# Optimization experiments

Measured on AMD Instinct MI355X. Metric: run time of the kernel, lower is better.

## Reference

```python
import jax, jax.numpy as jnp
import numpy as np

N = 50000        # nodes
E = 1_600_000    # edges (avg degree 32)
G = 512          # graphs
F_IN = 9         # node features
H = 64           # hidden dim
ED = 1           # edge feature dim


def _lin(k, fo, fi):
    w = jax.random.normal(k, (fo, fi), jnp.float32) * (1.0 / np.sqrt(fi))
    b = jnp.zeros((fo,), jnp.float32)
    return w, b


def setup_inputs() -> dict:
    key = jax.random.key(0)
    ks = jax.random.split(key, 16)
    x = jax.random.normal(ks[0], (N, F_IN), jnp.float32)
    edge_index = jax.random.randint(ks[1], (2, E), 0, N, dtype=jnp.int64)
    edge_attr = jax.random.normal(ks[2], (E, ED), jnp.float32)
    batch = jnp.sort(jax.random.randint(ks[3], (N,), 0, G, dtype=jnp.int64))
    B_total = jax.random.uniform(ks[4], (G,), jnp.float32) * 100.0
    terminal_mask = jax.random.randint(ks[5], (N,), 0, 2, dtype=jnp.int32)
    c_cost = jax.random.uniform(ks[6], (N,), jnp.float32)
    # conv1: edge lin (ED->F_IN), nn = Linear(F_IN,H), Linear(H,H)
    e1_w, e1_b = _lin(ks[7], F_IN, ED)
    w1a, b1a = _lin(ks[8], H, F_IN)
    w1b, b1b = _lin(ks[9], H, H)
    # conv2: edge lin (ED->H), nn = Linear(H,H), Linear(H,H)
    e2_w, e2_b = _lin(ks[10], H, ED)
    w2a, b2a = _lin(ks[11], H, H)
    w2b, b2b = _lin(ks[12], H, H)
    # readout: Linear(H,H//2), Linear(H//2,1)
    wr1, br1 = _lin(ks[13], H // 2, H)
    wr2, br2 = _lin(ks[14], 1, H // 2)
    return dict(x=x, edge_index=edge_index, edge_attr=edge_attr, batch=batch,
                B_total=B_total, terminal_mask=terminal_mask, c_cost=c_cost,
                e1_w=e1_w, e1_b=e1_b, w1a=w1a, b1a=b1a, w1b=w1b, b1b=b1b,
                e2_w=e2_w, e2_b=e2_b, w2a=w2a, b2a=b2a, w2b=w2b, b2b=b2b,
                wr1=wr1, br1=br1, wr2=wr2, br2=br2)


def _gine(x, src, dst, edge_attr, ew, eb, wa, ba, wb, bb):
    # GINEConv (eps=0): nn(x + sum_j relu(x_j + W_e e_ji))
    e = edge_attr @ ew.T + eb                    # [E, F]
    m = jax.nn.relu(x[src] + e)                  # [E, F] gather + edge fuse
    aggr = jax.ops.segment_sum(m, dst, num_segments=N)  # scatter-add -> [N, F]
    h = x + aggr
    h = jax.nn.relu(h @ wa.T + ba)
    h = jax.nn.relu(h @ wb.T + bb)
    return h


def reference(x, edge_index, edge_attr, batch, B_total, terminal_mask, c_cost,
              e1_w, e1_b, w1a, b1a, w1b, b1b,
              e2_w, e2_b, w2a, b2a, w2b, b2b,
              wr1, br1, wr2, br2):
    src, dst = edge_index[0], edge_index[1]
    h = _gine(x, src, dst, edge_attr, e1_w, e1_b, w1a, b1a, w1b, b1b)
    h = _gine(h, src, dst, edge_attr, e2_w, e2_b, w2a, b2a, w2b, b2b)
    pi_raw = jax.nn.sigmoid((jax.nn.relu(h @ wr1.T + br1) @ wr2.T + br2))[:, 0]
    pi_raw = pi_raw * (1.0 - terminal_mask.astype(jnp.float32))
    node_expenses = pi_raw * c_cost
    total_expenses = jax.ops.segment_sum(node_expenses, batch, num_segments=G)
    ratio = jnp.minimum(B_total[batch] / (total_expenses[batch] + 1e-12), 1.0)
    return pi_raw * ratio
```

## Files before the change

### kernel.cpp

```cpp
#include <hip/hip_runtime.h>
#include <hip/hip_fp16.h>
#include <math.h>

#define N_NODES 50000
#define N_EDGES 1600000
#define N_GRAPHS 512
#define F_IN 9
#define H 64
#define EPB 4096
#define N_SBLK ((N_EDGES + EPB - 1) / EPB)
#define BUCKET_NODES 64
#define N_FBUK ((N_NODES + BUCKET_NODES - 1) / BUCKET_NODES)
#define FCAP 2816

typedef _Float16 f16x8 __attribute__((ext_vector_type(8)));
typedef float f32x4 __attribute__((ext_vector_type(4)));
typedef float f32x2 __attribute__((ext_vector_type(2)));

__device__ __forceinline__ void pack_weights_body(
        const float* __restrict__ w1a, const float* __restrict__ w1b,
        const float* __restrict__ w2a, const float* __restrict__ w2b,
        const float* __restrict__ wr1,
        __half* __restrict__ pk1Ah, __half* __restrict__ pk1Al,
        __half* __restrict__ pk1Bh, __half* __restrict__ pk1Bl,
        __half* __restrict__ pkAh, __half* __restrict__ pkAl,
        __half* __restrict__ pkBh, __half* __restrict__ pkBl,
        __half* __restrict__ pkRh, __half* __restrict__ pkRl) {
    int t = threadIdx.x;
    for (int i = t; i < 2048; i += 512) {
        int j = i & 7, l = (i >> 3) & 63, tt = i >> 9;
        int q = l >> 4, n = l & 15;
        int k = q * 8 + j;
        float v = (k < F_IN) ? w1a[(tt * 16 + n) * F_IN + k] : 0.f;
        __half h = __float2half(v);
        pk1Ah[i] = h; pk1Al[i] = __float2half(v - __half2float(h));
    }
    for (int i = t; i < 4096; i += 512) {
        int j = i & 7, l = (i >> 3) & 63, c = (i >> 9) & 1, tt = i >> 10;
        int q = l >> 4, n = l & 15;
        int src = (tt * 16 + n) * H + c * 32 + q * 8 + j;
        float v1 = w1b[src], wa = w2a[src], wb = w2b[src];
        __half h1 = __float2half(v1), ah = __float2half(wa), bh = __float2half(wb);
        pk1Bh[i] = h1; pk1Bl[i] = __float2half(v1 - __half2float(h1));
        pkAh[i] = ah; pkAl[i] = __float2half(wa - __half2float(ah));
        pkBh[i] = bh; pkBl[i] = __float2half(wb - __half2float(bh));
    }
    for (int i = t; i < 2048; i += 512) {
        int j = i & 7, l = (i >> 3) & 63, c = (i >> 9) & 1, tt = i >> 10;
        int q = l >> 4, n = l & 15;
        float wr = wr1[(tt * 16 + n) * H + c * 32 + q * 8 + j];
        __half rh = __float2half(wr);
        pkRh[i] = rh; pkRl[i] = __float2half(wr - __half2float(rh));
    }
}

__global__ void __launch_bounds__(512)
bucket_scatter(const int* __restrict__ ei,
               const float* __restrict__ ea,
               int* __restrict__ bnext,
               uint2* __restrict__ ebuk,
               const float* __restrict__ w1a,
               const float* __restrict__ w1b,
               const float* __restrict__ w2a,
               const float* __restrict__ w2b,
               const float* __restrict__ wr1,
               __half* pk1Ah, __half* pk1Al,
               __half* pk1Bh, __half* pk1Bl,
               __half* pkAh, __half* pkAl,
               __half* pkBh, __half* pkBl,
               __half* pkRh, __half* pkRl) {
    if (blockIdx.x == 0) {
        pack_weights_body(w1a, w1b, w2a, w2b, wr1, pk1Ah, pk1Al, pk1Bh, pk1Bl,
                          pkAh, pkAl, pkBh, pkBl, pkRh, pkRl);
        return;
    }
    __shared__ int cnt[N_FBUK];
    __shared__ int gbase[N_FBUK];
    for (int i = threadIdx.x; i < N_FBUK; i += 512) cnt[i] = 0;
    __syncthreads();
    int base = (blockIdx.x - 1) * EPB;
    int rk[8];
    unsigned pay[8];
#pragma unroll
    for (int j = 0; j < 8; ++j) {
        int e = base + j * 512 + threadIdx.x;
        rk[j] = -1;
        if (e < N_EDGES) {
            int d = ei[N_EDGES + e];
            int s = ei[e];
            float a = ea[e];
            pay[j] = ((unsigned)s << 16) |
                     (unsigned)__half_as_ushort(__float2half(a));
            int b = d >> 6;
            int r = atomicAdd(&cnt[b], 1);
            rk[j] = (b << 19) | ((d & 63) << 13) | r;
        }
    }
    __syncthreads();
    for (int i = threadIdx.x; i < N_FBUK; i += 512)
        gbase[i] = cnt[i] ? atomicAdd(&bnext[i], cnt[i]) : 0;
    __syncthreads();
#pragma unroll
    for (int j = 0; j < 8; ++j) {
        if (rk[j] < 0) continue;
        int b = rk[j] >> 19, dl = (rk[j] >> 13) & 63, r = rk[j] & 8191;
        int slot = gbase[b] + r;
        if (slot >= FCAP) continue;
        ebuk[(size_t)b * FCAP + slot] = make_uint2(pay[j], (unsigned)dl);
    }
}

#define UNPACK_ATTR(P) __half2float(__ushort_as_half((unsigned short)((P) & 0xffffu)))

__device__ __forceinline__ void split8(const float* __restrict__ v,
                                       f16x8& hi, f16x8& lo) {
#pragma unroll
    for (int j = 0; j < 8; ++j) {
        _Float16 h = (_Float16)v[j];
        hi[j] = h;
        lo[j] = (_Float16)(v[j] - (float)h);
    }
}

#define TILE3(C, A0H, A0L, A1H, A1L, PH, PL, T) do {                          \
        f16x8 b0h = *(const f16x8*)((PH) + (((T) * 2 + 0) * 64 + lane) * 8);  \
        f16x8 b0l = *(const f16x8*)((PL) + (((T) * 2 + 0) * 64 + lane) * 8);  \
        f16x8 b1h = *(const f16x8*)((PH) + (((T) * 2 + 1) * 64 + lane) * 8);  \
        f16x8 b1l = *(const f16x8*)((PL) + (((T) * 2 + 1) * 64 + lane) * 8);  \
        C = __builtin_amdgcn_mfma_f32_16x16x32_f16(A0H, b0h, C, 0, 0, 0);     \
        C = __builtin_amdgcn_mfma_f32_16x16x32_f16(A0L, b0h, C, 0, 0, 0);     \
        C = __builtin_amdgcn_mfma_f32_16x16x32_f16(A0H, b0l, C, 0, 0, 0);     \
        C = __builtin_amdgcn_mfma_f32_16x16x32_f16(A1H, b1h, C, 0, 0, 0);     \
        C = __builtin_amdgcn_mfma_f32_16x16x32_f16(A1L, b1h, C, 0, 0, 0);     \
        C = __builtin_amdgcn_mfma_f32_16x16x32_f16(A1H, b1l, C, 0, 0, 0);     \
    } while (0)

__global__ void __launch_bounds__(512)
bucket_fine(const uint2* __restrict__ ebuk,
            const int* __restrict__ bnext,
            unsigned* __restrict__ ep4,
            int* __restrict__ starts, int* __restrict__ deg,
            const float* __restrict__ x,
            const float* __restrict__ e1w,
            const float* __restrict__ e1b,
            const __half* __restrict__ pk1Ah, const __half* __restrict__ pk1Al,
            const float* __restrict__ b1a,
            const __half* __restrict__ pk1Bh, const __half* __restrict__ pk1Bl,
            const float* __restrict__ b1b,
            __half* __restrict__ h1) {
    __shared__ unsigned sorted[FCAP];
    __shared__ int cntN[BUCKET_NODES], offN[BUCKET_NODES], nxtN[BUCKET_NODES];
    __shared__ float xs_lds[BUCKET_NODES][32];
    __shared__ float hbuf[4][16][68];
    int b = blockIdx.x;
    int base = b * FCAP;
    int count = bnext[b];
    if (count > FCAP) count = FCAP;
    int tid = threadIdx.x;
    if (tid < BUCKET_NODES) cntN[tid] = 0;
    __syncthreads();
    uint2 ev[6];
#pragma unroll
    for (int k = 0; k < 6; ++k) {
        int i = tid + k * 512;
        ev[k] = (i < count) ? ebuk[base + i] : make_uint2(0u, 0xFFFFFFFFu);
    }
#pragma unroll
    for (int k = 0; k < 6; ++k)
        if (ev[k].y < (unsigned)BUCKET_NODES) atomicAdd(&cntN[ev[k].y], 1);
    __syncthreads();
    if (tid < 64) {
        int v = cntN[tid];
        int incl = v;
#pragma unroll
        for (int off = 1; off < 64; off <<= 1) {
            int t = __shfl_up(incl, off, 64);
            if (tid >= off) incl += t;
        }
        int excl = incl - v;
        offN[tid] = excl;
        nxtN[tid] = 0;
        int n = (b << 6) + tid;
        if (n < N_NODES) { starts[n] = base + excl; deg[n] = v; }
    }
    __syncthreads();
#pragma unroll
    for (int k = 0; k < 6; ++k) {
        if (ev[k].y < (unsigned)BUCKET_NODES) {
            int r = atomicAdd(&nxtN[ev[k].y], 1);
            sorted[offN[ev[k].y] + r] = ev[k].x;
        }
    }
    __syncthreads();
    for (int i = tid; i < count; i += 512)
        ep4[base + i] = sorted[i];

    int lane = tid & 63, wid = tid >> 6;
    int slot = lane >> 4;
    int f = lane & 15;
    bool act = f < F_IN;
    float wf = act ? e1w[f] : 0.f;
    float bf = act ? e1b[f] : 0.f;
#pragma unroll
    for (int i = 0; i < 8; ++i) {
        int nloc = wid * 8 + i;
        int n = (b << 6) + nloc;
        bool valid = (n < N_NODES);
        int off = offN[nloc];
        int dgN = valid ? cntN[nloc] : 0;
        float acc = 0.f;
        int j = slot;
        for (; j + 12 < dgN; j += 16) {
            unsigned pa = sorted[off + j];
            unsigned pb = sorted[off + j + 4];
            unsigned pc = sorted[off + j + 8];
            unsigned pd = sorted[off + j + 12];
            float xa_ = act ? x[(pa >> 16) * F_IN + f] : 0.f;
            float xb_ = act ? x[(pb >> 16) * F_IN + f] : 0.f;
            float xc_ = act ? x[(pc >> 16) * F_IN + f] : 0.f;
            float xd_ = act ? x[(pd >> 16) * F_IN + f] : 0.f;
            if (act) {
                acc += fmaxf(xa_ + UNPACK_ATTR(pa) * wf + bf, 0.f)
                     + fmaxf(xb_ + UNPACK_ATTR(pb) * wf + bf, 0.f)
                     + fmaxf(xc_ + UNPACK_ATTR(pc) * wf + bf, 0.f)
                     + fmaxf(xd_ + UNPACK_ATTR(pd) * wf + bf, 0.f);
            }
        }
        for (; j < dgN; j += 4) {
            unsigned p = sorted[off + j];
            float xv = act ? x[(p >> 16) * F_IN + f] : 0.f;
            float m = xv + UNPACK_ATTR(p) * wf + bf;
            acc += act ? fmaxf(m, 0.f) : 0.f;
        }
        acc += __shfl_xor(acc, 16, 64);
        acc += __shfl_xor(acc, 32, 64);
        if (lane < 32) {
            float o = 0.f;
            if (valid && lane < F_IN) o = x[n * F_IN + lane] + acc;
            xs_lds[nloc][lane] = o;
        }
    }
    __syncthreads();

    bool mlpw = (wid < 4);
    int m = lane & 15, q = lane >> 4;
    const _Float16* pAh = (const _Float16*)pk1Ah;
    const _Float16* pAl = (const _Float16*)pk1Al;
    const _Float16* pBh = (const _Float16*)pk1Bh;
    const _Float16* pBl = (const _Float16*)pk1Bl;
    if (mlpw) {
        f16x8 ah, al;
        split8(&xs_lds[wid * 16 + m][q * 8], ah, al);
#pragma unroll
        for (int t = 0; t < 4; ++t) {
            f32x4 c = {0.f, 0.f, 0.f, 0.f};
            f16x8 bh = *(const f16x8*)(pAh + (t * 64 + lane) * 8);
            f16x8 bl = *(const f16x8*)(pAl + (t * 64 + lane) * 8);
            c = __builtin_amdgcn_mfma_f32_16x16x32_f16(ah, bh, c, 0, 0, 0);
            c = __builtin_amdgcn_mfma_f32_16x16x32_f16(al, bh, c, 0, 0, 0);
            c = __builtin_amdgcn_mfma_f32_16x16x32_f16(ah, bl, c, 0, 0, 0);
            float bias = b1a[t * 16 + m];
#pragma unroll
            for (int r = 0; r < 4; ++r)
                hbuf[wid][q * 4 + r][t * 16 + m] = fmaxf(c[r] + bias, 0.f);
        }
    }
    __syncthreads();
    if (mlpw) {
        f16x8 a0h, a0l, a1h, a1l;
        split8(&hbuf[wid][m][q * 8], a0h, a0l);
        split8(&hbuf[wid][m][32 + q * 8], a1h, a1l);
        float tmp[4][4];
#pragma unroll
        for (int t = 0; t < 4; ++t) {
            f32x4 c = {0.f, 0.f, 0.f, 0.f};
            TILE3(c, a0h, a0l, a1h, a1l, pBh, pBl, t);
            float bias = b1b[t * 16 + m];
#pragma unroll
            for (int r = 0; r < 4; ++r)
                tmp[t][r] = fmaxf(c[r] + bias, 0.f);
        }
        __builtin_amdgcn_s_barrier();
#pragma unroll
        for (int t = 0; t < 4; ++t)
#pragma unroll
            for (int r = 0; r < 4; ++r)
                hbuf[wid][q * 4 + r][t * 16 + m] = tmp[t][r];
        int nn = lane >> 2, part = lane & 3;
        int n = (b << 6) + wid * 16 + nn;
        if (n < N_NODES) {
            f16x8 vlo, vhi;
            const float* rlo = &hbuf[wid][nn][part * 8];
            const float* rhi = &hbuf[wid][nn][32 + part * 8];
#pragma unroll
            for (int j = 0; j < 8; ++j) {
                vlo[j] = (_Float16)rlo[j];
                vhi[j] = (_Float16)rhi[j];
            }
            *(f16x8*)(h1 + (size_t)n * 64 + part * 8) = vlo;
            *(f16x8*)(h1 + (size_t)n * 64 + 32 + part * 8) = vhi;
        }
    }
}

__global__ void aggphase2_kernel(const __half* __restrict__ h1,
                                 const int* __restrict__ starts,
                                 const int* __restrict__ deg,
                                 const unsigned* __restrict__ ep4,
                                 const float* __restrict__ ew,
                                 const float* __restrict__ eb,
                                 float* __restrict__ htot) {
    int n = blockIdx.x * (blockDim.x >> 6) + (threadIdx.x >> 6);
    int lane = threadIdx.x & 63;
    if (n >= N_NODES) return;
    int q = lane >> 4;
    int l = lane & 15;
    int s0 = starts[n], dg = deg[n];
    const unsigned* ep = ep4 + s0;
    const uint2* h1v = (const uint2*)h1;
    float4 w4 = *(const float4*)(ew + 4 * l);
    float4 b4 = *(const float4*)(eb + 4 * l);
    float a0 = 0.f, a1 = 0.f, a2 = 0.f, a3 = 0.f;
#define EDGE4(P, V) do {                                                   \
        float at = UNPACK_ATTR(P);                                         \
        float2 lo = __half22float2(*(const __half2*)&(V).x);               \
        float2 hi = __half22float2(*(const __half2*)&(V).y);               \
        a0 += fmaxf(lo.x + at * w4.x + b4.x, 0.f);                         \
        a1 += fmaxf(lo.y + at * w4.y + b4.y, 0.f);                         \
        a2 += fmaxf(hi.x + at * w4.z + b4.z, 0.f);                         \
        a3 += fmaxf(hi.y + at * w4.w + b4.w, 0.f);                         \
    } while (0)
    int j = 0;
    for (; j + 16 <= dg; j += 16) {
        unsigned p0 = ep[j + q], p1 = ep[j + 4 + q];
        unsigned p2 = ep[j + 8 + q], p3 = ep[j + 12 + q];
        uint2 v0 = h1v[(size_t)(p0 >> 16) * 16 + l];
        uint2 v1 = h1v[(size_t)(p1 >> 16) * 16 + l];
        uint2 v2 = h1v[(size_t)(p2 >> 16) * 16 + l];
        uint2 v3 = h1v[(size_t)(p3 >> 16) * 16 + l];
        EDGE4(p0, v0); EDGE4(p1, v1); EDGE4(p2, v2); EDGE4(p3, v3);
    }
    for (; j + 4 <= dg; j += 4) {
        unsigned p = ep[j + q];
        uint2 v = h1v[(size_t)(p >> 16) * 16 + l];
        EDGE4(p, v);
    }
    int rem = dg - j;
    if (q < rem) {
        unsigned p = ep[j + q];
        uint2 v = h1v[(size_t)(p >> 16) * 16 + l];
        EDGE4(p, v);
    }
#undef EDGE4
    a0 += __shfl_xor(a0, 16, 64); a0 += __shfl_xor(a0, 32, 64);
    a1 += __shfl_xor(a1, 16, 64); a1 += __shfl_xor(a1, 32, 64);
    a2 += __shfl_xor(a2, 16, 64); a2 += __shfl_xor(a2, 32, 64);
    a3 += __shfl_xor(a3, 16, 64); a3 += __shfl_xor(a3, 32, 64);
    if (q == 0) {
        uint2 sv = h1v[(size_t)n * 16 + l];
        float2 lo = __half22float2(*(const __half2*)&sv.x);
        float2 hi = __half22float2(*(const __half2*)&sv.y);
        f32x4 o;
        o[0] = lo.x + a0; o[1] = lo.y + a1; o[2] = hi.x + a2; o[3] = hi.y + a3;
        __builtin_nontemporal_store(o, (f32x4*)(htot + (size_t)n * 64 + 4 * l));
    }
}

__global__ void node2_kernel(const float* __restrict__ htot,
                             const __half* __restrict__ pkAh, const __half* __restrict__ pkAl,
                             const float* __restrict__ b2a,
                             const __half* __restrict__ pkBh, const __half* __restrict__ pkBl,
                             const float* __restrict__ b2b,
                             const __half* __restrict__ pkRh, const __half* __restrict__ pkRl,
                             const float* __restrict__ br1,
                             const float* __restrict__ wr2,
                             const float* __restrict__ br2,
                             const int* __restrict__ term,
                             const int* __restrict__ batch,
                             const float* __restrict__ ccost,
                             float* __restrict__ pi,
                             float* __restrict__ te) {
    __shared__ float hbuf[4][16][68];
    int wv = threadIdx.x >> 6;
    int lane = threadIdx.x & 63;
    int gwave = blockIdx.x * 4 + wv;
    bool active = gwave < (N_NODES / 16);
    int base = active ? gwave * 16 : 0;
    int m = lane & 15, q = lane >> 4;
    const _Float16* pAh = (const _Float16*)pkAh;
    const _Float16* pAl = (const _Float16*)pkAl;
    const _Float16* pBh = (const _Float16*)pkBh;
    const _Float16* pBl = (const _Float16*)pkBl;
    const _Float16* pRh = (const _Float16*)pkRh;
    const _Float16* pRl = (const _Float16*)pkRl;

    f16x8 a0h, a0l, a1h, a1l;
    {
        const float* hrow = htot + (size_t)(base + m) * 64;
        split8(hrow + q * 8, a0h, a0l);
        split8(hrow + 32 + q * 8, a1h, a1l);
    }
#pragma unroll
    for (int t = 0; t < 4; ++t) {
        f32x4 c = {0.f, 0.f, 0.f, 0.f};
        TILE3(c, a0h, a0l, a1h, a1l, pAh, pAl, t);
        float bias = b2a[t * 16 + m];
#pragma unroll
        for (int r = 0; r < 4; ++r)
            hbuf[wv][q * 4 + r][t * 16 + m] = fmaxf(c[r] + bias, 0.f);
    }
    __syncthreads();
    split8(&hbuf[wv][m][q * 8], a0h, a0l);
    split8(&hbuf[wv][m][32 + q * 8], a1h, a1l);
    float tmp[4][4];
#pragma unroll
    for (int t = 0; t < 4; ++t) {
        f32x4 c = {0.f, 0.f, 0.f, 0.f};
        TILE3(c, a0h, a0l, a1h, a1l, pBh, pBl, t);
        float bias = b2b[t * 16 + m];
#pragma unroll
        for (int r = 0; r < 4; ++r)
            tmp[t][r] = fmaxf(c[r] + bias, 0.f);
    }
    __syncthreads();
#pragma unroll
    for (int t = 0; t < 4; ++t)
#pragma unroll
        for (int r = 0; r < 4; ++r)
            hbuf[wv][q * 4 + r][t * 16 + m] = tmp[t][r];
    __syncthreads();
    split8(&hbuf[wv][m][q * 8], a0h, a0l);
    split8(&hbuf[wv][m][32 + q * 8], a1h, a1l);
    float partial[4] = {0.f, 0.f, 0.f, 0.f};
#pragma unroll
    for (int t = 0; t < 2; ++t) {
        f32x4 c = {0.f, 0.f, 0.f, 0.f};
        TILE3(c, a0h, a0l, a1h, a1l, pRh, pRl, t);
        float bias = br1[t * 16 + m];
        float wv2 = wr2[t * 16 + m];
#pragma unroll
        for (int r = 0; r < 4; ++r)
            partial[r] += fmaxf(c[r] + bias, 0.f) * wv2;
    }
#pragma unroll
    for (int off = 1; off < 16; off <<= 1) {
        partial[0] += __shfl_xor(partial[0], off, 64);
        partial[1] += __shfl_xor(partial[1], off, 64);
        partial[2] += __shfl_xor(partial[2], off, 64);
        partial[3] += __shfl_xor(partial[3], off, 64);
    }
    if (active && m == 0) {
#pragma unroll
        for (int r = 0; r < 4; ++r) {
            int n = base + q * 4 + r;
            float z = partial[r] + br2[0];
            float sig = 1.f / (1.f + expf(-z));
            float pv = sig * (1.f - (float)term[n]);
            pi[n] = pv;
            float contrib = pv * ccost[n];
            if (contrib != 0.f) atomicAdd(&te[batch[n]], contrib);
        }
    }
}

__global__ void final_kernel(const float* __restrict__ pi,
                             const int* __restrict__ batch,
                             const float* __restrict__ Btot,
                             const float* __restrict__ te,
                             float* __restrict__ out) {
    int n = blockIdx.x * blockDim.x + threadIdx.x;
    if (n >= N_NODES) return;
    int b = batch[n];
    float ratio = fminf(Btot[b] / (te[b] + 1e-12f), 1.f);
    out[n] = pi[n] * ratio;
}

extern "C" void kernel_launch(void* const* d_in, const int* in_sizes, int n_in,
                              void* d_out, int out_size, void* d_ws, size_t ws_size,
                              hipStream_t stream) {
    const float* x     = (const float*)d_in[0];
    const int*   ei    = (const int*)d_in[1];
    const float* ea    = (const float*)d_in[2];
    const int*   batch = (const int*)d_in[3];
    const float* Btot  = (const float*)d_in[4];
    const int*   term  = (const int*)d_in[5];
    const float* ccost = (const float*)d_in[6];
    const float* e1w   = (const float*)d_in[7];
    const float* e1b   = (const float*)d_in[8];
    const float* w1a   = (const float*)d_in[9];
    const float* b1a   = (const float*)d_in[10];
    const float* w1b   = (const float*)d_in[11];
    const float* b1b   = (const float*)d_in[12];
    const float* e2w   = (const float*)d_in[13];
    const float* e2b   = (const float*)d_in[14];
    const float* w2a   = (const float*)d_in[15];
    const float* b2a   = (const float*)d_in[16];
    const float* w2b   = (const float*)d_in[17];
    const float* b2b   = (const float*)d_in[18];
    const float* wr1   = (const float*)d_in[19];
    const float* br1   = (const float*)d_in[20];
    const float* wr2   = (const float*)d_in[21];
    const float* br2   = (const float*)d_in[22];

    char* p = (char*)d_ws;
    int*      bnext  = (int*)p;      p += sizeof(int)      * 1024;
    float*    te     = (float*)p;    p += sizeof(float)    * N_GRAPHS;
    int*      starts = (int*)p;      p += sizeof(int)      * N_NODES;
    int*      deg    = (int*)p;      p += sizeof(int)      * N_NODES;
    p = (char*)(((size_t)p + 15) & ~(size_t)15);
    uint2*    ebuk   = (uint2*)p;    p += sizeof(uint2)    * (size_t)N_FBUK * FCAP;
    unsigned* ep4    = (unsigned*)p; p += sizeof(unsigned) * (size_t)N_FBUK * FCAP;
    __half*   h1     = (__half*)p;   p += sizeof(__half)   * (size_t)N_NODES * 64;
    float*    htot   = (float*)p;    p += sizeof(float)    * (size_t)N_NODES * 64;
    float*    pi     = (float*)p;    p += sizeof(float)    * N_NODES;
    __half*   pk1Ah  = (__half*)p;   p += sizeof(__half)   * 2048;
    __half*   pk1Al  = (__half*)p;   p += sizeof(__half)   * 2048;
    __half*   pk1Bh  = (__half*)p;   p += sizeof(__half)   * 4096;
    __half*   pk1Bl  = (__half*)p;   p += sizeof(__half)   * 4096;
    __half*   pkAh   = (__half*)p;   p += sizeof(__half)   * 4096;
    __half*   pkAl   = (__half*)p;   p += sizeof(__half)   * 4096;
    __half*   pkBh   = (__half*)p;   p += sizeof(__half)   * 4096;
    __half*   pkBl   = (__half*)p;   p += sizeof(__half)   * 4096;
    __half*   pkRh   = (__half*)p;   p += sizeof(__half)   * 2048;
    __half*   pkRl   = (__half*)p;   p += sizeof(__half)   * 2048;
    float*    out    = (float*)d_out;

    hipMemsetAsync(d_ws, 0, sizeof(int) * 1024 + sizeof(float) * N_GRAPHS, stream);

    bucket_scatter<<<1 + N_SBLK, 512, 0, stream>>>(ei, ea, bnext, ebuk,
                                                   w1a, w1b, w2a, w2b, wr1,
                                                   pk1Ah, pk1Al, pk1Bh, pk1Bl,
                                                   pkAh, pkAl, pkBh, pkBl, pkRh, pkRl);
    bucket_fine<<<N_FBUK, 512, 0, stream>>>(ebuk, bnext, ep4, starts, deg,
                                            x, e1w, e1b,
                                            pk1Ah, pk1Al, b1a, pk1Bh, pk1Bl, b1b, h1);
    aggphase2_kernel<<<(N_NODES + 3) / 4, 256, 0, stream>>>(h1, starts, deg, ep4,
                                                            e2w, e2b, htot);
    node2_kernel<<<(N_NODES / 16 + 3) / 4, 256, 0, stream>>>(htot,
                                                             pkAh, pkAl, b2a,
                                                             pkBh, pkBl, b2b,
                                                             pkRh, pkRl, br1,
                                                             wr2, br2, term,
                                                             batch, ccost, pi, te);
    final_kernel<<<(N_NODES + 255) / 256, 256, 0, stream>>>(pi, batch, Btot, te, out);
}
```

Before: 217.3 us.

## Fuse layer-2 aggregation with node MLP and readout via LDS staging

```diff
diff --git a/kernel.cpp b/kernel.cpp
--- a/kernel.cpp
+++ b/kernel.cpp
@@ -264,9 +264,6 @@
             for (int r = 0; r < 4; ++r)
                 hbuf[wid][q * 4 + r][t * 16 + m] = fmaxf(c[r] + bias, 0.f);
         }
-    }
-    __syncthreads();
-    if (mlpw) {
         f16x8 a0h, a0l, a1h, a1l;
         split8(&hbuf[wid][m][q * 8], a0h, a0l);
         split8(&hbuf[wid][m][32 + q * 8], a1h, a1l);
@@ -280,7 +277,6 @@
             for (int r = 0; r < 4; ++r)
                 tmp[t][r] = fmaxf(c[r] + bias, 0.f);
         }
-        __builtin_amdgcn_s_barrier();
 #pragma unroll
         for (int t = 0; t < 4; ++t)
 #pragma unroll
@@ -303,24 +299,35 @@
     }
 }
 
-__global__ void aggphase2_kernel(const __half* __restrict__ h1,
-                                 const int* __restrict__ starts,
-                                 const int* __restrict__ deg,
-                                 const unsigned* __restrict__ ep4,
-                                 const float* __restrict__ ew,
-                                 const float* __restrict__ eb,
-                                 float* __restrict__ htot) {
-    int n = blockIdx.x * (blockDim.x >> 6) + (threadIdx.x >> 6);
-    int lane = threadIdx.x & 63;
-    if (n >= N_NODES) return;
+__global__ void __launch_bounds__(256)
+aggnode2_kernel(const __half* __restrict__ h1,
+                const int* __restrict__ starts,
+                const int* __restrict__ deg,
+                const unsigned* __restrict__ ep4,
+                const float* __restrict__ ew,
+                const float* __restrict__ eb,
+                const __half* __restrict__ pkAh, const __half* __restrict__ pkAl,
+                const float* __restrict__ b2a,
+                const __half* __restrict__ pkBh, const __half* __restrict__ pkBl,
+                const float* __restrict__ b2b,
+                const __half* __restrict__ pkRh, const __half* __restrict__ pkRl,
+                const float* __restrict__ br1,
+                const float* __restrict__ wr2,
+                const float* __restrict__ br2,
+                const int* __restrict__ term,
+                const int* __restrict__ batch,
+                const float* __restrict__ ccost,
+                float* __restrict__ pi,
+                float* __restrict__ te) {
+    __shared__ float htot_lds[16][68];
+    __shared__ float hbuf[16][68];
+    int lane = threadIdx.x & 63, wid = threadIdx.x >> 6;
+    int gbase = blockIdx.x * 16;
     int q = lane >> 4;
     int l = lane & 15;
-    int s0 = starts[n], dg = deg[n];
-    const unsigned* ep = ep4 + s0;
     const uint2* h1v = (const uint2*)h1;
     float4 w4 = *(const float4*)(ew + 4 * l);
     float4 b4 = *(const float4*)(eb + 4 * l);
-    float a0 = 0.f, a1 = 0.f, a2 = 0.f, a3 = 0.f;
 #define EDGE4(P, V) do {                                                   \
         float at = UNPACK_ATTR(P);                                         \
         float2 lo = __half22float2(*(const __half2*)&(V).x);               \
@@ -330,135 +337,118 @@
         a2 += fmaxf(hi.x + at * w4.z + b4.z, 0.f);                         \
         a3 += fmaxf(hi.y + at * w4.w + b4.w, 0.f);                         \
     } while (0)
-    int j = 0;
-    for (; j + 16 <= dg; j += 16) {
-        unsigned p0 = ep[j + q], p1 = ep[j + 4 + q];
-        unsigned p2 = ep[j + 8 + q], p3 = ep[j + 12 + q];
-        uint2 v0 = h1v[(size_t)(p0 >> 16) * 16 + l];
-        uint2 v1 = h1v[(size_t)(p1 >> 16) * 16 + l];
-        uint2 v2 = h1v[(size_t)(p2 >> 16) * 16 + l];
-        uint2 v3 = h1v[(size_t)(p3 >> 16) * 16 + l];
-        EDGE4(p0, v0); EDGE4(p1, v1); EDGE4(p2, v2); EDGE4(p3, v3);
-    }
-    for (; j + 4 <= dg; j += 4) {
-        unsigned p = ep[j + q];
-        uint2 v = h1v[(size_t)(p >> 16) * 16 + l];
-        EDGE4(p, v);
-    }
-    int rem = dg - j;
-    if (q < rem) {
-        unsigned p = ep[j + q];
-        uint2 v = h1v[(size_t)(p >> 16) * 16 + l];
-        EDGE4(p, v);
+#pragma unroll
+    for (int k = 0; k < 4; ++k) {
+        int nloc = wid * 4 + k;
+        int n = gbase + nloc;
+        int s0 = starts[n], dg = deg[n];
+        const unsigned* ep = ep4 + s0;
+        float a0 = 0.f, a1 = 0.f, a2 = 0.f, a3 = 0.f;
+        int j = 0;
+        for (; j + 16 <= dg; j += 16) {
+            unsigned p0 = ep[j + q], p1 = ep[j + 4 + q];
+            unsigned p2 = ep[j + 8 + q], p3 = ep[j + 12 + q];
+            uint2 v0 = h1v[(size_t)(p0 >> 16) * 16 + l];
+            uint2 v1 = h1v[(size_t)(p1 >> 16) * 16 + l];
+            uint2 v2 = h1v[(size_t)(p2 >> 16) * 16 + l];
+            uint2 v3 = h1v[(size_t)(p3 >> 16) * 16 + l];
+            EDGE4(p0, v0); EDGE4(p1, v1); EDGE4(p2, v2); EDGE4(p3, v3);
+        }
+        for (; j + 4 <= dg; j += 4) {
+            unsigned p = ep[j + q];
+            uint2 v = h1v[(size_t)(p >> 16) * 16 + l];
+            EDGE4(p, v);
+        }
+        int rem = dg - j;
+        if (q < rem) {
+            unsigned p = ep[j + q];
+            uint2 v = h1v[(size_t)(p >> 16) * 16 + l];
+            EDGE4(p, v);
+        }
+        a0 += __shfl_xor(a0, 16, 64); a0 += __shfl_xor(a0, 32, 64);
+        a1 += __shfl_xor(a1, 16, 64); a1 += __shfl_xor(a1, 32, 64);
+        a2 += __shfl_xor(a2, 16, 64); a2 += __shfl_xor(a2, 32, 64);
+        a3 += __shfl_xor(a3, 16, 64); a3 += __shfl_xor(a3, 32, 64);
+        if (q == 0) {
+            uint2 sv = h1v[(size_t)n * 16 + l];
+            float2 lo = __half22float2(*(const __half2*)&sv.x);
+            float2 hi = __half22float2(*(const __half2*)&sv.y);
+            f32x4 o;
+            o[0] = lo.x + a0; o[1] = lo.y + a1; o[2] = hi.x + a2; o[3] = hi.y + a3;
+            *(f32x4*)&htot_lds[nloc][4 * l] = o;
+        }
     }
 #undef EDGE4
-    a0 += __shfl_xor(a0, 16, 64); a0 += __shfl_xor(a0, 32, 64);
-    a1 += __shfl_xor(a1, 16, 64); a1 += __shfl_xor(a1, 32, 64);
-    a2 += __shfl_xor(a2, 16, 64); a2 += __shfl_xor(a2, 32, 64);
-    a3 += __shfl_xor(a3, 16, 64); a3 += __shfl_xor(a3, 32, 64);
-    if (q == 0) {
-        uint2 sv = h1v[(size_t)n * 16 + l];
-        float2 lo = __half22float2(*(const __half2*)&sv.x);
-        float2 hi = __half22float2(*(const __half2*)&sv.y);
-        f32x4 o;
-        o[0] = lo.x + a0; o[1] = lo.y + a1; o[2] = hi.x + a2; o[3] = hi.y + a3;
-        __builtin_nontemporal_store(o, (f32x4*)(htot + (size_t)n * 64 + 4 * l));
-    }
-}
-
-__global__ void node2_kernel(const float* __restrict__ htot,
-                             const __half* __restrict__ pkAh, const __half* __restrict__ pkAl,
-                             const float* __restrict__ b2a,
-                             const __half* __restrict__ pkBh, const __half* __restrict__ pkBl,
-                             const float* __restrict__ b2b,
-                             const __half* __restrict__ pkRh, const __half* __restrict__ pkRl,
-                             const float* __restrict__ br1,
-                             const float* __restrict__ wr2,
-                             const float* __restrict__ br2,
-                             const int* __restrict__ term,
-                             const int* __restrict__ batch,
-                             const float* __restrict__ ccost,
-                             float* __restrict__ pi,
-                             float* __restrict__ te) {
-    __shared__ float hbuf[4][16][68];
-    int wv = threadIdx.x >> 6;
-    int lane = threadIdx.x & 63;
-    int gwave = blockIdx.x * 4 + wv;
-    bool active = gwave < (N_NODES / 16);
-    int base = active ? gwave * 16 : 0;
-    int m = lane & 15, q = lane >> 4;
-    const _Float16* pAh = (const _Float16*)pkAh;
-    const _Float16* pAl = (const _Float16*)pkAl;
-    const _Float16* pBh = (const _Float16*)pkBh;
-    const _Float16* pBl = (const _Float16*)pkBl;
-    const _Float16* pRh = (const _Float16*)pkRh;
-    const _Float16* pRl = (const _Float16*)pkRl;
-
-    f16x8 a0h, a0l, a1h, a1l;
-    {
-        const float* hrow = htot + (size_t)(base + m) * 64;
-        split8(hrow + q * 8, a0h, a0l);
-        split8(hrow + 32 + q * 8, a1h, a1l);
-    }
-#pragma unroll
-    for (int t = 0; t < 4; ++t) {
-        f32x4 c = {0.f, 0.f, 0.f, 0.f};
-        TILE3(c, a0h, a0l, a1h, a1l, pAh, pAl, t);
-        float bias = b2a[t * 16 + m];
-#pragma unroll
-        for (int r = 0; r < 4; ++r)
-            hbuf[wv][q * 4 + r][t * 16 + m] = fmaxf(c[r] + bias, 0.f);
-    }
-    __syncthreads();
-    split8(&hbuf[wv][m][q * 8], a0h, a0l);
-    split8(&hbuf[wv][m][32 + q * 8], a1h, a1l);
-    float tmp[4][4];
-#pragma unroll
-    for (int t = 0; t < 4; ++t) {
-        f32x4 c = {0.f, 0.f, 0.f, 0.f};
-        TILE3(c, a0h, a0l, a1h, a1l, pBh, pBl, t);
-        float bias = b2b[t * 16 + m];
-#pragma unroll
-        for (int r = 0; r < 4; ++r)
-            tmp[t][r] = fmaxf(c[r] + bias, 0.f);
-    }
-    __syncthreads();
-#pragma unroll
-    for (int t = 0; t < 4; ++t)
-#pragma unroll
-        for (int r = 0; r < 4; ++r)
-            hbuf[wv][q * 4 + r][t * 16 + m] = tmp[t][r];
-    __syncthreads();
-    split8(&hbuf[wv][m][q * 8], a0h, a0l);
-    split8(&hbuf[wv][m][32 + q * 8], a1h, a1l);
-    float partial[4] = {0.f, 0.f, 0.f, 0.f};
-#pragma unroll
-    for (int t = 0; t < 2; ++t) {
-        f32x4 c = {0.f, 0.f, 0.f, 0.f};
-        TILE3(c, a0h, a0l, a1h, a1l, pRh, pRl, t);
-        float bias = br1[t * 16 + m];
-        float wv2 = wr2[t * 16 + m];
-#pragma unroll
-        for (int r = 0; r < 4; ++r)
-            partial[r] += fmaxf(c[r] + bias, 0.f) * wv2;
-    }
-#pragma unroll
-    for (int off = 1; off < 16; off <<= 1) {
-        partial[0] += __shfl_xor(partial[0], off, 64);
-        partial[1] += __shfl_xor(partial[1], off, 64);
-        partial[2] += __shfl_xor(partial[2], off, 64);
-        partial[3] += __shfl_xor(partial[3], off, 64);
-    }
-    if (active && m == 0) {
-#pragma unroll
-        for (int r = 0; r < 4; ++r) {
-            int n = base + q * 4 + r;
-            float z = partial[r] + br2[0];
-            float sig = 1.f / (1.f + expf(-z));
-            float pv = sig * (1.f - (float)term[n]);
-            pi[n] = pv;
-            float contrib = pv * ccost[n];
-            if (contrib != 0.f) atomicAdd(&te[batch[n]], contrib);
+    __syncthreads();
+
+    if (wid == 0) {
+        int m = lane & 15;
+        const _Float16* pAh = (const _Float16*)pkAh;
+        const _Float16* pAl = (const _Float16*)pkAl;
+        const _Float16* pBh = (const _Float16*)pkBh;
+        const _Float16* pBl = (const _Float16*)pkBl;
+        const _Float16* pRh = (const _Float16*)pkRh;
+        const _Float16* pRl = (const _Float16*)pkRl;
+        f16x8 a0h, a0l, a1h, a1l;
+        split8(&htot_lds[m][q * 8], a0h, a0l);
+        split8(&htot_lds[m][32 + q * 8], a1h, a1l);
+#pragma unroll
+        for (int t = 0; t < 4; ++t) {
+            f32x4 c = {0.f, 0.f, 0.f, 0.f};
+            TILE3(c, a0h, a0l, a1h, a1l, pAh, pAl, t);
+            float bias = b2a[t * 16 + m];
+#pragma unroll
+            for (int r = 0; r < 4; ++r)
+                hbuf[q * 4 + r][t * 16 + m] = fmaxf(c[r] + bias, 0.f);
+        }
+        split8(&hbuf[m][q * 8], a0h, a0l);
+        split8(&hbuf[m][32 + q * 8], a1h, a1l);
+        float tmp[4][4];
+#pragma unroll
+        for (int t = 0; t < 4; ++t) {
+            f32x4 c = {0.f, 0.f, 0.f, 0.f};
+            TILE3(c, a0h, a0l, a1h, a1l, pBh, pBl, t);
+            float bias = b2b[t * 16 + m];
+#pragma unroll
+            for (int r = 0; r < 4; ++r)
+                tmp[t][r] = fmaxf(c[r] + bias, 0.f);
+        }
+#pragma unroll
+        for (int t = 0; t < 4; ++t)
+#pragma unroll
+            for (int r = 0; r < 4; ++r)
+                hbuf[q * 4 + r][t * 16 + m] = tmp[t][r];
+        split8(&hbuf[m][q * 8], a0h, a0l);
+        split8(&hbuf[m][32 + q * 8], a1h, a1l);
+        float partial[4] = {0.f, 0.f, 0.f, 0.f};
+#pragma unroll
+        for (int t = 0; t < 2; ++t) {
+            f32x4 c = {0.f, 0.f, 0.f, 0.f};
+            TILE3(c, a0h, a0l, a1h, a1l, pRh, pRl, t);
+            float bias = br1[t * 16 + m];
+            float wv2 = wr2[t * 16 + m];
+#pragma unroll
+            for (int r = 0; r < 4; ++r)
+                partial[r] += fmaxf(c[r] + bias, 0.f) * wv2;
+        }
+#pragma unroll
+        for (int off = 1; off < 16; off <<= 1) {
+            partial[0] += __shfl_xor(partial[0], off, 64);
+            partial[1] += __shfl_xor(partial[1], off, 64);
+            partial[2] += __shfl_xor(partial[2], off, 64);
+            partial[3] += __shfl_xor(partial[3], off, 64);
+        }
+        if (m == 0) {
+#pragma unroll
+            for (int r = 0; r < 4; ++r) {
+                int n = gbase + q * 4 + r;
+                float z = partial[r] + br2[0];
+                float sig = 1.f / (1.f + expf(-z));
+                float pv = sig * (1.f - (float)term[n]);
+                pi[n] = pv;
+                float contrib = pv * ccost[n];
+                if (contrib != 0.f) atomicAdd(&te[batch[n]], contrib);
+            }
         }
     }
 }
@@ -511,7 +501,6 @@
     uint2*    ebuk   = (uint2*)p;    p += sizeof(uint2)    * (size_t)N_FBUK * FCAP;
     unsigned* ep4    = (unsigned*)p; p += sizeof(unsigned) * (size_t)N_FBUK * FCAP;
     __half*   h1     = (__half*)p;   p += sizeof(__half)   * (size_t)N_NODES * 64;
-    float*    htot   = (float*)p;    p += sizeof(float)    * (size_t)N_NODES * 64;
     float*    pi     = (float*)p;    p += sizeof(float)    * N_NODES;
     __half*   pk1Ah  = (__half*)p;   p += sizeof(__half)   * 2048;
     __half*   pk1Al  = (__half*)p;   p += sizeof(__half)   * 2048;
@@ -534,13 +523,12 @@
     bucket_fine<<<N_FBUK, 512, 0, stream>>>(ebuk, bnext, ep4, starts, deg,
                                             x, e1w, e1b,
                                             pk1Ah, pk1Al, b1a, pk1Bh, pk1Bl, b1b, h1);
-    aggphase2_kernel<<<(N_NODES + 3) / 4, 256, 0, stream>>>(h1, starts, deg, ep4,
-                                                            e2w, e2b, htot);
-    node2_kernel<<<(N_NODES / 16 + 3) / 4, 256, 0, stream>>>(htot,
-                                                             pkAh, pkAl, b2a,
-                                                             pkBh, pkBl, b2b,
-                                                             pkRh, pkRl, br1,
-                                                             wr2, br2, term,
-                                                             batch, ccost, pi, te);
+    aggnode2_kernel<<<N_NODES / 16, 256, 0, stream>>>(h1, starts, deg, ep4,
+                                                      e2w, e2b,
+                                                      pkAh, pkAl, b2a,
+                                                      pkBh, pkBl, b2b,
+                                                      pkRh, pkRl, br1,
+                                                      wr2, br2, term,
+                                                      batch, ccost, pi, te);
     final_kernel<<<(N_NODES + 255) / 256, 256, 0, stream>>>(pi, batch, Btot, te, out);
 }
```

Measured after the change: 248.8 us. 1.14x slower.
